# Kernel optimization log

Hardware: AMD Instinct MI355X
Metric: run time of the kernel (lower is better)

## Reference

```python
import jax, jax.numpy as jnp
import numpy as np

B, T, F, H, NH, L = 32, 512, 16, 64, 4, 2
HD = H // NH


def _ln(x, g, b, eps=1e-5):
    m = x.mean(-1, keepdims=True)
    v = ((x - m) ** 2).mean(-1, keepdims=True)
    return (x - m) / jnp.sqrt(v + eps) * g + b


def _glu(x, w, b):
    a, g = jnp.split(x @ w + b, 2, axis=-1)
    return a * jax.nn.sigmoid(g)


def _lstm_layer(x, w_ih, w_hh, b):
    # x: (B,T,H); PyTorch gate order i,f,g,o
    Bd = x.shape[0]

    def step(carry, xt):
        h, c = carry
        gates = xt @ w_ih + h @ w_hh + b
        i, f, g, o = jnp.split(gates, 4, axis=-1)
        c = jax.nn.sigmoid(f) * c + jax.nn.sigmoid(i) * jnp.tanh(g)
        h = jax.nn.sigmoid(o) * jnp.tanh(c)
        return (h, c), h

    z = jnp.zeros((Bd, H), x.dtype)
    _, hs = jax.lax.scan(step, (z, z), jnp.swapaxes(x, 0, 1))
    return jnp.swapaxes(hs, 0, 1)


def setup_inputs() -> dict:
    key = jax.random.key(0)
    specs = [
        ("x", (B, T, F), "n"),
        ("ip_w", (H,), "n"), ("ip_b", (H,), "n"),
        ("vsn_fc1_w", (F, H, H), "n"), ("vsn_fc1_b", (F, H), "n"),
        ("vsn_fc2_w", (F, H, 2 * H), "n"), ("vsn_fc2_b", (F, 2 * H), "n"),
        ("vsn_ln_g", (F, H), "1"), ("vsn_ln_b", (F, H), "0"),
        ("sel_fc1_w", (F * H, H), "n"), ("sel_fc1_b", (H,), "n"),
        ("sel_fc2_w", (H, 2 * F), "n"), ("sel_fc2_b", (2 * F,), "n"),
        ("sel_skip_w", (F * H, F), "n"), ("sel_skip_b", (F,), "n"),
        ("sel_ln_g", (F,), "1"), ("sel_ln_b", (F,), "0"),
        ("lstm_w_ih", (L, H, 4 * H), "n"), ("lstm_w_hh", (L, H, 4 * H), "n"), ("lstm_b", (L, 4 * H), "n"),
        ("plg_w", (H, 2 * H), "n"), ("plg_b", (2 * H,), "n"),
        ("pln_g", (H,), "1"), ("pln_b", (H,), "0"),
        ("qkv_w", (H, 3 * H), "n"), ("qkv_b", (3 * H,), "n"),
        ("ao_w", (H, H), "n"), ("ao_b", (H,), "n"),
        ("pag_w", (H, 2 * H), "n"), ("pag_b", (2 * H,), "n"),
        ("pan_g", (H,), "1"), ("pan_b", (H,), "0"),
        ("ff1_w", (H, 4 * H), "n"), ("ff1_b", (4 * H,), "n"),
        ("ff2_w", (4 * H, 2 * H), "n"), ("ff2_b", (2 * H,), "n"),
        ("ffln_g", (H,), "1"), ("ffln_b", (H,), "0"),
        ("fn_g", (H,), "1"), ("fn_b", (H,), "0"),
        ("out_w", (H, 1), "n"), ("out_b", (1,), "n"),
    ]
    keys = jax.random.split(key, len(specs))
    d = {}
    for (name, shp, kind), k in zip(specs, keys):
        if kind == "n":
            scale = 1.0 if name == "x" else 0.05
            d[name] = jax.random.normal(k, shp, jnp.float32) * scale
        elif kind == "1":
            d[name] = jnp.ones(shp, jnp.float32)
        else:
            d[name] = jnp.zeros(shp, jnp.float32)
    return d


def reference(x, ip_w, ip_b, vsn_fc1_w, vsn_fc1_b, vsn_fc2_w, vsn_fc2_b, vsn_ln_g, vsn_ln_b,
              sel_fc1_w, sel_fc1_b, sel_fc2_w, sel_fc2_b, sel_skip_w, sel_skip_b, sel_ln_g, sel_ln_b,
              lstm_w_ih, lstm_w_hh, lstm_b, plg_w, plg_b, pln_g, pln_b,
              qkv_w, qkv_b, ao_w, ao_b, pag_w, pag_b, pan_g, pan_b,
              ff1_w, ff1_b, ff2_w, ff2_b, ffln_g, ffln_b, fn_g, fn_b, out_w, out_b):
    Bd, Td, Fd = x.shape
    # input_proj: Linear(1,H) applied to each scalar feature -> (B,T,F,H)
    xp = x[..., None] * ip_w + ip_b
    # --- VSN (vectorized over B and T; torch loops over T and F) ---
    flat = xp.reshape(Bd, Td, Fd * H)
    h = jax.nn.elu(flat @ sel_fc1_w + sel_fc1_b)
    a, g = jnp.split(h @ sel_fc2_w + sel_fc2_b, 2, axis=-1)
    sel = _ln(a * jax.nn.sigmoid(g) + (flat @ sel_skip_w + sel_skip_b), sel_ln_g, sel_ln_b)
    w = jax.nn.softmax(sel, axis=-1)  # (B,T,F)
    h = jax.nn.elu(jnp.einsum('btfi,fio->btfo', xp, vsn_fc1_w) + vsn_fc1_b)
    a, g = jnp.split(jnp.einsum('btfi,fio->btfo', h, vsn_fc2_w) + vsn_fc2_b, 2, axis=-1)
    proc = _ln(a * jax.nn.sigmoid(g) + xp, vsn_ln_g, vsn_ln_b)  # (B,T,F,H)
    vsn_out = jnp.einsum('btf,btfh->bth', w, proc)
    # --- 2-layer LSTM encoder (dropout inactive in eval) ---
    seq = vsn_out
    for l in range(L):
        seq = _lstm_layer(seq, lstm_w_ih[l], lstm_w_hh[l], lstm_b[l])
    lo = _ln(_glu(seq, plg_w, plg_b) + vsn_out, pln_g, pln_b)
    # --- self-attention ---
    q, k, v = jnp.split(lo @ qkv_w + qkv_b, 3, axis=-1)
    q = q.reshape(Bd, Td, NH, HD)
    k = k.reshape(Bd, Td, NH, HD)
    v = v.reshape(Bd, Td, NH, HD)
    sc = jnp.einsum('bqhd,bkhd->bhqk', q, k) / jnp.sqrt(jnp.float32(HD))
    att = jnp.einsum('bhqk,bkhd->bqhd', jax.nn.softmax(sc, axis=-1), v).reshape(Bd, Td, H)
    att = att @ ao_w + ao_b
    at = _ln(_glu(att, pag_w, pag_b) + lo, pan_g, pan_b)
    # --- FF GRN + final norm ---
    h = jax.nn.elu(at @ ff1_w + ff1_b)
    a, g = jnp.split(h @ ff2_w + ff2_b, 2, axis=-1)
    ff = _ln(a * jax.nn.sigmoid(g) + at, ffln_g, ffln_b)
    ff = _ln(ff + at, fn_g, fn_b)
    return ff[:, -1, :] @ out_w + out_b  # (B, forecast_horizon)
```

## Files before the change

kernel.cpp:

```cpp
#include <hip/hip_runtime.h>
#include <math.h>


__device__ __forceinline__ float sigf(float x){
    return 1.f / (1.f + __expf(-x));
}
__device__ __forceinline__ float tanhf_(float x){
    float xc = fminf(fmaxf(x, -15.f), 15.f);
    float e = __expf(-2.f * xc);
    return (1.f - e) / (1.f + e);
}
__device__ __forceinline__ float eluf(float x){
    return x > 0.f ? x : (__expf(x) - 1.f);
}
__device__ __forceinline__ float wsum64(float v){
    #pragma unroll
    for (int o = 1; o < 64; o <<= 1) v += __shfl_xor(v, o, 64);
    return v;
}
__device__ __forceinline__ float wmax64(float v){
    #pragma unroll
    for (int o = 1; o < 64; o <<= 1) v = fmaxf(v, __shfl_xor(v, o, 64));
    return v;
}

#define BARRIER_LGKM() do {                                    \
    asm volatile("s_waitcnt lgkmcnt(0)" ::: "memory");         \
    __builtin_amdgcn_s_barrier();                              \
} while(0)

__global__ __launch_bounds__(256) void tft_vsn_kernel(
    const float* __restrict__ x,
    const float* __restrict__ ip_w, const float* __restrict__ ip_b,
    const float* __restrict__ vfc1w, const float* __restrict__ vfc1b,
    const float* __restrict__ vfc2w, const float* __restrict__ vfc2b,
    const float* __restrict__ vlng, const float* __restrict__ vlnb,
    const float* __restrict__ sfc1w, const float* __restrict__ sfc1b,
    const float* __restrict__ sfc2w, const float* __restrict__ sfc2b,
    const float* __restrict__ sskw, const float* __restrict__ sskb,
    const float* __restrict__ slng, const float* __restrict__ slnb,
    float* __restrict__ vsn_out)
{
    __shared__ __align__(16) float s_x[512];
    __shared__ __align__(16) float s_ipw[64];
    __shared__ __align__(16) float s_ipb[64];
    __shared__ __align__(16) float s_xp[32*65];
    __shared__ __align__(16) float s_W1[64*64];
    __shared__ __align__(16) float s_W2[64*128];
    __shared__ __align__(16) float s_Wsk[64*16];
    __shared__ __align__(16) float s_h[32*65];
    __shared__ __align__(16) float s_sel2[32*32];
    __shared__ __align__(16) float s_wsm[32*16];
    __shared__ __align__(16) float s_lng[64];
    __shared__ __align__(16) float s_lnb[64];
    __shared__ __align__(16) float s_b1[64];
    __shared__ __align__(16) float s_b2[128];

    const int tid  = threadIdx.x;
    const int pos0 = blockIdx.x * 32;
    const int m    = tid >> 3;
    const int g8   = tid & 7;
    const int j0   = g8 * 8;

    if (tid < 128) ((float4*)s_x)[tid] = *(const float4*)(x + pos0*16 + tid*4);
    if (tid < 64) { s_ipw[tid] = ip_w[tid]; s_ipb[tid] = ip_b[tid]; }
    __syncthreads();

    float accS[8];
    #pragma unroll
    for (int i = 0; i < 8; i++) accS[i] = 0.f;
    float accK0 = 0.f, accK1 = 0.f;

    for (int f = 0; f < 16; f++){
        {
            float xb = s_x[m*16 + f];
            #pragma unroll
            for (int i = 0; i < 8; i++)
                s_xp[m*65 + j0 + i] = xb * s_ipw[j0+i] + s_ipb[j0+i];
        }
        #pragma unroll
        for (int i = 0; i < 4; i++)
            ((float4*)s_W1)[tid + i*256] = *(const float4*)(sfc1w + f*4096 + (tid + i*256)*4);
        ((float4*)s_Wsk)[tid] = *(const float4*)(sskw + f*1024 + tid*4);
        __syncthreads();
        #pragma unroll 8
        for (int k = 0; k < 64; k++){
            float xv = s_xp[m*65 + k];
            const float4* wr = (const float4*)(s_W1 + k*64 + j0);
            float4 w0 = wr[0], w1 = wr[1];
            accS[0] += xv*w0.x; accS[1] += xv*w0.y; accS[2] += xv*w0.z; accS[3] += xv*w0.w;
            accS[4] += xv*w1.x; accS[5] += xv*w1.y; accS[6] += xv*w1.z; accS[7] += xv*w1.w;
            float2 wk = *(const float2*)(s_Wsk + k*16 + g8*2);
            accK0 += xv*wk.x; accK1 += xv*wk.y;
        }
        __syncthreads();
    }

    #pragma unroll
    for (int i = 0; i < 8; i++)
        s_h[m*65 + j0 + i] = eluf(accS[i] + sfc1b[j0+i]);
    ((float4*)s_W1)[tid]       = *(const float4*)(sfc2w + tid*4);
    ((float4*)s_W1)[tid + 256] = *(const float4*)(sfc2w + 1024 + tid*4);
    __syncthreads();

    {
        const int jj = g8 * 4;
        float a0 = 0.f, a1 = 0.f, a2 = 0.f, a3 = 0.f;
        #pragma unroll 8
        for (int k = 0; k < 64; k++){
            float hv = s_h[m*65 + k];
            float4 w = *(const float4*)(s_W1 + k*32 + jj);
            a0 += hv*w.x; a1 += hv*w.y; a2 += hv*w.z; a3 += hv*w.w;
        }
        s_sel2[m*32 + jj+0] = a0 + sfc2b[jj+0];
        s_sel2[m*32 + jj+1] = a1 + sfc2b[jj+1];
        s_sel2[m*32 + jj+2] = a2 + sfc2b[jj+2];
        s_sel2[m*32 + jj+3] = a3 + sfc2b[jj+3];
    }
    __syncthreads();

    {
        const int f0 = g8 * 2;
        float a0 = s_sel2[m*32 + f0],   g0 = s_sel2[m*32 + 16 + f0];
        float a1 = s_sel2[m*32 + f0+1], g1 = s_sel2[m*32 + 16 + f0+1];
        float pre0 = a0*sigf(g0) + accK0 + sskb[f0];
        float pre1 = a1*sigf(g1) + accK1 + sskb[f0+1];
        float sum = pre0 + pre1;
        sum += __shfl_xor(sum,1,8); sum += __shfl_xor(sum,2,8); sum += __shfl_xor(sum,4,8);
        float mean = sum * 0.0625f;
        float d0 = pre0 - mean, d1 = pre1 - mean;
        float vv = d0*d0 + d1*d1;
        vv += __shfl_xor(vv,1,8); vv += __shfl_xor(vv,2,8); vv += __shfl_xor(vv,4,8);
        float rstd = rsqrtf(vv * 0.0625f + 1e-5f);
        float sv0 = d0*rstd*slng[f0]   + slnb[f0];
        float sv1 = d1*rstd*slng[f0+1] + slnb[f0+1];
        float mx = fmaxf(sv0, sv1);
        mx = fmaxf(mx, __shfl_xor(mx,1,8));
        mx = fmaxf(mx, __shfl_xor(mx,2,8));
        mx = fmaxf(mx, __shfl_xor(mx,4,8));
        float e0 = __expf(sv0 - mx), e1 = __expf(sv1 - mx);
        float es = e0 + e1;
        es += __shfl_xor(es,1,8); es += __shfl_xor(es,2,8); es += __shfl_xor(es,4,8);
        float inv = 1.f / es;
        s_wsm[m*16 + f0]   = e0 * inv;
        s_wsm[m*16 + f0+1] = e1 * inv;
    }
    __syncthreads();

    float accV[8];
    #pragma unroll
    for (int i = 0; i < 8; i++) accV[i] = 0.f;

    for (int f = 0; f < 16; f++){
        {
            float xb = s_x[m*16 + f];
            #pragma unroll
            for (int i = 0; i < 8; i++)
                s_xp[m*65 + j0 + i] = xb * s_ipw[j0+i] + s_ipb[j0+i];
        }
        #pragma unroll
        for (int i = 0; i < 4; i++)
            ((float4*)s_W1)[tid + i*256] = *(const float4*)(vfc1w + f*4096 + (tid + i*256)*4);
        #pragma unroll
        for (int i = 0; i < 8; i++)
            ((float4*)s_W2)[tid + i*256] = *(const float4*)(vfc2w + f*8192 + (tid + i*256)*4);
        if (tid < 16)       ((float4*)s_b1)[tid]     = *(const float4*)(vfc1b + f*64  + tid*4);
        else if (tid < 48)  ((float4*)s_b2)[tid-16]  = *(const float4*)(vfc2b + f*128 + (tid-16)*4);
        else if (tid < 64)  ((float4*)s_lng)[tid-48] = *(const float4*)(vlng  + f*64  + (tid-48)*4);
        else if (tid < 80)  ((float4*)s_lnb)[tid-64] = *(const float4*)(vlnb  + f*64  + (tid-64)*4);
        __syncthreads();

        float ah[8];
        #pragma unroll
        for (int i = 0; i < 8; i++) ah[i] = 0.f;
        #pragma unroll 8
        for (int k = 0; k < 64; k++){
            float xv = s_xp[m*65 + k];
            const float4* wr = (const float4*)(s_W1 + k*64 + j0);
            float4 w0 = wr[0], w1 = wr[1];
            ah[0] += xv*w0.x; ah[1] += xv*w0.y; ah[2] += xv*w0.z; ah[3] += xv*w0.w;
            ah[4] += xv*w1.x; ah[5] += xv*w1.y; ah[6] += xv*w1.z; ah[7] += xv*w1.w;
        }
        #pragma unroll
        for (int i = 0; i < 8; i++)
            s_h[m*65 + j0 + i] = eluf(ah[i] + s_b1[j0+i]);
        __syncthreads();

        float aa[8], ag[8];
        #pragma unroll
        for (int i = 0; i < 8; i++){ aa[i] = 0.f; ag[i] = 0.f; }
        #pragma unroll 4
        for (int k = 0; k < 64; k++){
            float hv = s_h[m*65 + k];
            const float4* war = (const float4*)(s_W2 + k*128 + j0);
            const float4* wgr = (const float4*)(s_W2 + k*128 + 64 + j0);
            float4 wa0 = war[0], wa1 = war[1];
            float4 wg0 = wgr[0], wg1 = wgr[1];
            aa[0] += hv*wa0.x; aa[1] += hv*wa0.y; aa[2] += hv*wa0.z; aa[3] += hv*wa0.w;
            aa[4] += hv*wa1.x; aa[5] += hv*wa1.y; aa[6] += hv*wa1.z; aa[7] += hv*wa1.w;
            ag[0] += hv*wg0.x; ag[1] += hv*wg0.y; ag[2] += hv*wg0.z; ag[3] += hv*wg0.w;
            ag[4] += hv*wg1.x; ag[5] += hv*wg1.y; ag[6] += hv*wg1.z; ag[7] += hv*wg1.w;
        }
        float pre[8];
        float lsum = 0.f;
        #pragma unroll
        for (int i = 0; i < 8; i++){
            float av = aa[i] + s_b2[j0+i];
            float gv = ag[i] + s_b2[64 + j0+i];
            pre[i] = av * sigf(gv) + s_xp[m*65 + j0 + i];
            lsum += pre[i];
        }
        lsum += __shfl_xor(lsum,1,8); lsum += __shfl_xor(lsum,2,8); lsum += __shfl_xor(lsum,4,8);
        float mean = lsum * 0.015625f;
        float lvar = 0.f;
        #pragma unroll
        for (int i = 0; i < 8; i++){ float d = pre[i] - mean; lvar += d*d; }
        lvar += __shfl_xor(lvar,1,8); lvar += __shfl_xor(lvar,2,8); lvar += __shfl_xor(lvar,4,8);
        float rstd = rsqrtf(lvar * 0.015625f + 1e-5f);
        float wf = s_wsm[m*16 + f];
        #pragma unroll
        for (int i = 0; i < 8; i++)
            accV[i] += wf * ((pre[i] - mean) * rstd * s_lng[j0+i] + s_lnb[j0+i]);
        __syncthreads();
    }

    float4 o0 = make_float4(accV[0], accV[1], accV[2], accV[3]);
    float4 o1 = make_float4(accV[4], accV[5], accV[6], accV[7]);
    *(float4*)(vsn_out + (pos0 + m)*64 + j0)     = o0;
    *(float4*)(vsn_out + (pos0 + m)*64 + j0 + 4) = o1;
}

__global__ __launch_bounds__(256) void tft_xgates_kernel(
    const float* __restrict__ vsn, const float* __restrict__ w_ih,
    const float* __restrict__ bias, float* __restrict__ gpre)
{
    __shared__ __align__(16) float s_w[64*256];
    __shared__ __align__(16) float s_vT[64*20];
    __shared__ __align__(16) float s_b[256];
    const int tid  = threadIdx.x;
    const int pos0 = blockIdx.x * 16;

    #pragma unroll
    for (int i = 0; i < 16; i++)
        ((float4*)s_w)[tid + i*256] = *(const float4*)(w_ih + (tid + i*256)*4);
    s_b[tid] = bias[tid];
    {
        int mm = tid >> 4;
        int k0 = (tid & 15) * 4;
        float4 v = *(const float4*)(vsn + (pos0 + mm)*64 + k0);
        s_vT[(k0+0)*20 + mm] = v.x;
        s_vT[(k0+1)*20 + mm] = v.y;
        s_vT[(k0+2)*20 + mm] = v.z;
        s_vT[(k0+3)*20 + mm] = v.w;
    }
    __syncthreads();

    float acc[16];
    #pragma unroll
    for (int i = 0; i < 16; i++) acc[i] = 0.f;
    #pragma unroll 8
    for (int k = 0; k < 64; k++){
        float wv = s_w[k*256 + tid];
        const float4* vr = (const float4*)(s_vT + k*20);
        float4 v0 = vr[0], v1 = vr[1], v2 = vr[2], v3 = vr[3];
        acc[0]  += wv*v0.x; acc[1]  += wv*v0.y; acc[2]  += wv*v0.z; acc[3]  += wv*v0.w;
        acc[4]  += wv*v1.x; acc[5]  += wv*v1.y; acc[6]  += wv*v1.z; acc[7]  += wv*v1.w;
        acc[8]  += wv*v2.x; acc[9]  += wv*v2.y; acc[10] += wv*v2.z; acc[11] += wv*v2.w;
        acc[12] += wv*v3.x; acc[13] += wv*v3.y; acc[14] += wv*v3.z; acc[15] += wv*v3.w;
    }
    float bv = s_b[tid];
    #pragma unroll
    for (int i = 0; i < 16; i++)
        gpre[(pos0 + i)*256 + tid] = acc[i] + bv;
}

#define LW(P, c) make_float4((P)[(4*(c)+0)*256], (P)[(4*(c)+1)*256], \
                             (P)[(4*(c)+2)*256], (P)[(4*(c)+3)*256])

#define ACC(c, hv) { float4 h_ = (hv);                                      \
    a0  += h_.x*WA_##c.x; a0x += h_.y*WA_##c.y;                             \
    a0  += h_.z*WA_##c.z; a0x += h_.w*WA_##c.w;                             \
    a1  += h_.x*WB_##c.x; a1x += h_.y*WB_##c.y;                             \
    a1  += h_.z*WB_##c.z; a1x += h_.w*WB_##c.w; }

__global__ __launch_bounds__(512, 1) void tft_lstm_kernel(
    const float* __restrict__ w_ih, const float* __restrict__ w_hh,
    const float* __restrict__ bias, const float* __restrict__ gpre,
    float* __restrict__ seq)
{
    __shared__ __align__(16) float s_h1[2][64];
    __shared__ __align__(16) float s_h2[2][64];

    const int tid   = threadIdx.x;
    const int b     = blockIdx.x;
    const int lane  = tid & 63;
    const int wid   = tid >> 6;
    const int role  = wid >> 2;
    const int j     = ((wid & 3) << 4) | (lane & 15);
    const int kh    = (lane >> 4) & 1;
    const int gpair = (lane >> 5) & 1;
    const bool sub0 = (lane & 48) == 0;

    const int g0 = (gpair ? 64 : 0) + j;
    const int g1 = (gpair ? 192 : 128) + j;

    const float* bA;
    const float* bB;
    if (role == 0){
        bA = w_hh + (kh * 32) * 256 + g0;
        bB = w_hh + (kh * 32) * 256 + g1;
    } else {
        const float* mat = kh ? (w_hh + 16384) : (w_ih + 16384);
        bA = mat + g0;
        bB = mat + g1;
    }
    const float4 z4 = make_float4(0.f, 0.f, 0.f, 0.f);
    float4 WA_0 = LW(bA,0), WA_1 = LW(bA,1), WA_2 = LW(bA,2), WA_3 = LW(bA,3);
    float4 WA_4 = LW(bA,4), WA_5 = LW(bA,5), WA_6 = LW(bA,6), WA_7 = LW(bA,7);
    float4 WB_0 = LW(bB,0), WB_1 = LW(bB,1), WB_2 = LW(bB,2), WB_3 = LW(bB,3);
    float4 WB_4 = LW(bB,4), WB_5 = LW(bB,5), WB_6 = LW(bB,6), WB_7 = LW(bB,7);
    float4 WA_8 = z4, WA_9 = z4, WA_10 = z4, WA_11 = z4;
    float4 WA_12 = z4, WA_13 = z4, WA_14 = z4, WA_15 = z4;
    float4 WB_8 = z4, WB_9 = z4, WB_10 = z4, WB_11 = z4;
    float4 WB_12 = z4, WB_13 = z4, WB_14 = z4, WB_15 = z4;
    if (role == 1){
        WA_8  = LW(bA,8);  WA_9  = LW(bA,9);  WA_10 = LW(bA,10); WA_11 = LW(bA,11);
        WA_12 = LW(bA,12); WA_13 = LW(bA,13); WA_14 = LW(bA,14); WA_15 = LW(bA,15);
        WB_8  = LW(bB,8);  WB_9  = LW(bB,9);  WB_10 = LW(bB,10); WB_11 = LW(bB,11);
        WB_12 = LW(bB,12); WB_13 = LW(bB,13); WB_14 = LW(bB,14); WB_15 = LW(bB,15);
    }

    const float b2A = (role == 1 && kh == 0) ? bias[256 + g0] : 0.f;
    const float b2B = (role == 1 && kh == 0) ? bias[256 + g1] : 0.f;

    const bool gpl = (role == 0 && kh == 0);
    const float* gpbA = gpre + (size_t)b * 131072 + g0;
    const float* gpbB = gpre + (size_t)b * 131072 + g1;
    float gA0 = 0.f, gA1 = 0.f, gA2 = 0.f;
    float gB0 = 0.f, gB1 = 0.f, gB2 = 0.f;
    if (gpl){
        gA0 = gpbA[0];   gB0 = gpbB[0];
        gA1 = gpbA[256]; gB1 = gpbB[256];
        gA2 = gpbA[512]; gB2 = gpbB[512];
    }

    if (tid < 64){ s_h1[0][tid] = 0.f; s_h1[1][tid] = 0.f; }
    else if (tid < 128){ s_h2[0][tid-64] = 0.f; s_h2[1][tid-64] = 0.f; }
    float c_ = 0.f;
    __syncthreads();

    float* rd1 = &s_h1[1][0]; float* wr1 = &s_h1[0][0];
    float* rd2 = &s_h2[1][0]; float* wr2 = &s_h2[0][0];
    float* seqb = seq + (size_t)b * 512 * 64;

    for (int n = 0; n <= 512; ++n){
        float a0  = (role == 0) ? gA0 : b2A;
        float a1  = (role == 0) ? gB0 : b2B;
        float a0x = 0.f, a1x = 0.f;
        if (role == 0){
            const float4* hp = (const float4*)rd1 + kh * 8;
            ACC(0, hp[0]) ACC(1, hp[1]) ACC(2, hp[2]) ACC(3, hp[3])
            ACC(4, hp[4]) ACC(5, hp[5]) ACC(6, hp[6]) ACC(7, hp[7])
        } else {
            const float4* hp = (const float4*)(kh ? rd2 : rd1);
            ACC(0, hp[0])  ACC(1, hp[1])  ACC(2, hp[2])  ACC(3, hp[3])
            ACC(4, hp[4])  ACC(5, hp[5])  ACC(6, hp[6])  ACC(7, hp[7])
            ACC(8, hp[8])  ACC(9, hp[9])  ACC(10,hp[10]) ACC(11,hp[11])
            ACC(12,hp[12]) ACC(13,hp[13]) ACC(14,hp[14]) ACC(15,hp[15])
        }
        float A0 = a0 + a0x;
        float A1 = a1 + a1x;
        A0 += __shfl_xor(A0, 16, 64);
        A1 += __shfl_xor(A1, 16, 64);
        float B0 = __shfl_xor(A0, 32, 64);
        float B1 = __shfl_xor(A1, 32, 64);
        float gi = gpair ? B0 : A0;
        float gf = gpair ? A0 : B0;
        float gg = gpair ? B1 : A1;
        float go = gpair ? A1 : B1;

        if (role == 0){
            if (n < 512){
                c_ = sigf(gf)*c_ + sigf(gi)*tanhf_(gg);
                float h1v = sigf(go)*tanhf_(c_);
                if (sub0) wr1[j] = h1v;
            }
            if (gpl){
                gA0 = gA1; gA1 = gA2;
                gB0 = gB1; gB1 = gB2;
                if (n + 3 < 512){ gA2 = gpbA[(n+3)*256]; gB2 = gpbB[(n+3)*256]; }
            }
        } else if (n >= 1){
            c_ = sigf(gf)*c_ + sigf(gi)*tanhf_(gg);
            float h2v = sigf(go)*tanhf_(c_);
            if (sub0){
                wr2[j] = h2v;
                seqb[(size_t)(n-1)*64 + j] = h2v;
            }
        }
        BARRIER_LGKM();
        float* t1 = rd1; rd1 = wr1; wr1 = t1;
        float* t2 = rd2; rd2 = wr2; wr2 = t2;
    }
}

__global__ __launch_bounds__(256) void tft_lokv_kernel(
    const float* __restrict__ seq, const float* __restrict__ vsn,
    const float* __restrict__ plgw, const float* __restrict__ plgb,
    const float* __restrict__ png,  const float* __restrict__ pnb,
    const float* __restrict__ qkvw, const float* __restrict__ qkvb,
    float* __restrict__ kbuf, float* __restrict__ vbuf,
    float* __restrict__ qlast, float* __restrict__ lolast)
{
    __shared__ __align__(16) float s_pw[64*128];
    __shared__ __align__(16) float s_qw[64*192];
    __shared__ __align__(16) float s_pb[128];
    __shared__ __align__(16) float s_png[64];
    __shared__ __align__(16) float s_pnb[64];
    __shared__ __align__(16) float s_qb[192];
    __shared__ __align__(16) float s_row[4][64];
    __shared__ __align__(16) float s_lo[4][64];

    const int tid  = threadIdx.x;
    const int lane = tid & 63;
    const int wid  = tid >> 6;

    #pragma unroll
    for (int i = 0; i < 8; i++)
        ((float4*)s_pw)[tid + i*256] = *(const float4*)(plgw + (tid + i*256)*4);
    #pragma unroll
    for (int i = 0; i < 12; i++)
        ((float4*)s_qw)[tid + i*256] = *(const float4*)(qkvw + (tid + i*256)*4);
    if (tid < 128) s_pb[tid] = plgb[tid];
    if (tid < 64){ s_png[tid] = png[tid]; s_pnb[tid] = pnb[tid]; }
    if (tid < 192) s_qb[tid] = qkvb[tid];
    __syncthreads();

    for (int it = 0; it < 16; it++){
        int mpos = blockIdx.x*64 + wid*16 + it;
        int b = mpos >> 9, t = mpos & 511;
        float sv = seq[mpos*64 + lane];
        float vs = vsn[mpos*64 + lane];
        s_row[wid][lane] = sv;
        __syncthreads();
        float a = s_pb[lane], g = s_pb[64 + lane];
        #pragma unroll 8
        for (int k = 0; k < 64; k++){
            float rv = s_row[wid][k];
            a += rv * s_pw[k*128 + lane];
            g += rv * s_pw[k*128 + 64 + lane];
        }
        float pre = a * sigf(g) + vs;
        float mean = wsum64(pre) * 0.015625f;
        float d = pre - mean;
        float vv = wsum64(d*d) * 0.015625f;
        float lo = d * rsqrtf(vv + 1e-5f) * s_png[lane] + s_pnb[lane];
        s_lo[wid][lane] = lo;
        __syncthreads();
        float ka = s_qb[64 + lane], va = s_qb[128 + lane];
        #pragma unroll 8
        for (int k = 0; k < 64; k++){
            float lv = s_lo[wid][k];
            ka += lv * s_qw[k*192 + 64 + lane];
            va += lv * s_qw[k*192 + 128 + lane];
        }
        int h = lane >> 4, dd = lane & 15;
        kbuf[((b*4 + h)*512 + t)*16 + dd] = ka;
        vbuf[((b*4 + h)*512 + t)*16 + dd] = va;
        if (t == 511){
            float qa = s_qb[lane];
            #pragma unroll 8
            for (int k = 0; k < 64; k++)
                qa += s_lo[wid][k] * s_qw[k*192 + lane];
            qlast[b*64 + lane] = qa;
            lolast[b*64 + lane] = lo;
        }
    }
}

__global__ __launch_bounds__(256) void tft_head_kernel(
    const float* __restrict__ kbuf, const float* __restrict__ vbuf,
    const float* __restrict__ qlast, const float* __restrict__ lolast,
    const float* __restrict__ aow,  const float* __restrict__ aob,
    const float* __restrict__ pagw, const float* __restrict__ pagb,
    const float* __restrict__ pang, const float* __restrict__ panb,
    const float* __restrict__ ff1w, const float* __restrict__ ff1b,
    const float* __restrict__ ff2w, const float* __restrict__ ff2b,
    const float* __restrict__ fflng, const float* __restrict__ fflnb,
    const float* __restrict__ fng,  const float* __restrict__ fnb,
    const float* __restrict__ outw, const float* __restrict__ outb,
    float* __restrict__ out)
{
    __shared__ __align__(16) float s_q[64];
    __shared__ __align__(16) float s_lo[64];
    __shared__ __align__(16) float s_sc[4*512];
    __shared__ __align__(16) float s_part[4][64];
    __shared__ __align__(16) float s_a[64];
    __shared__ __align__(16) float s_a2[64];
    __shared__ __align__(16) float s_z[128];
    __shared__ __align__(16) float s_at[64];
    __shared__ __align__(16) float s_f1[256];

    const int tid = threadIdx.x;
    const int b   = blockIdx.x;
    if (tid < 64){ s_q[tid] = qlast[b*64 + tid]; s_lo[tid] = lolast[b*64 + tid]; }
    __syncthreads();

    for (int idx = tid; idx < 2048; idx += 256){
        int h = idx >> 9, t = idx & 511;
        const float4* kr = (const float4*)(kbuf + ((b*4 + h)*512 + t)*16);
        const float4* qr = (const float4*)(s_q + h*16);
        float4 k0 = kr[0], k1 = kr[1], k2 = kr[2], k3 = kr[3];
        float4 q0 = qr[0], q1 = qr[1], q2 = qr[2], q3 = qr[3];
        float d = q0.x*k0.x + q0.y*k0.y + q0.z*k0.z + q0.w*k0.w
                + q1.x*k1.x + q1.y*k1.y + q1.z*k1.z + q1.w*k1.w
                + q2.x*k2.x + q2.y*k2.y + q2.z*k2.z + q2.w*k2.w
                + q3.x*k3.x + q3.y*k3.y + q3.z*k3.z + q3.w*k3.w;
        s_sc[idx] = d * 0.25f;
    }
    __syncthreads();
    {
        int h = tid >> 6, lane = tid & 63;
        float v[8];
        float mx = -1e30f;
        #pragma unroll
        for (int j = 0; j < 8; j++){ v[j] = s_sc[h*512 + lane + j*64]; mx = fmaxf(mx, v[j]); }
        mx = wmax64(mx);
        float sum = 0.f;
        #pragma unroll
        for (int j = 0; j < 8; j++){ v[j] = __expf(v[j] - mx); sum += v[j]; }
        sum = wsum64(sum);
        float inv = 1.f / sum;
        #pragma unroll
        for (int j = 0; j < 8; j++) s_sc[h*512 + lane + j*64] = v[j] * inv;
    }
    __syncthreads();
    {
        int j = tid & 63, part = tid >> 6;
        int h = j >> 4, dd = j & 15;
        float pa = 0.f;
        for (int t = part*128; t < (part+1)*128; t++)
            pa += s_sc[h*512 + t] * vbuf[((b*4 + h)*512 + t)*16 + dd];
        s_part[part][j] = pa;
    }
    __syncthreads();
    if (tid < 64) s_a[tid] = s_part[0][tid] + s_part[1][tid] + s_part[2][tid] + s_part[3][tid];
    __syncthreads();
    if (tid < 64){
        float o = aob[tid];
        #pragma unroll 8
        for (int k = 0; k < 64; k++) o += s_a[k] * aow[k*64 + tid];
        s_a2[tid] = o;
    }
    __syncthreads();
    if (tid < 128){
        float z = pagb[tid];
        #pragma unroll 8
        for (int k = 0; k < 64; k++) z += s_a2[k] * pagw[k*128 + tid];
        s_z[tid] = z;
    }
    __syncthreads();
    if (tid < 64){
        float pre = s_z[tid] * sigf(s_z[64 + tid]) + s_lo[tid];
        float mean = wsum64(pre) * 0.015625f;
        float d = pre - mean;
        float vv = wsum64(d*d) * 0.015625f;
        s_at[tid] = d * rsqrtf(vv + 1e-5f) * pang[tid] + panb[tid];
    }
    __syncthreads();
    {
        float hv = ff1b[tid];
        #pragma unroll 8
        for (int k = 0; k < 64; k++) hv += s_at[k] * ff1w[k*256 + tid];
        s_f1[tid] = eluf(hv);
    }
    __syncthreads();
    if (tid < 128){
        float z = ff2b[tid];
        #pragma unroll 8
        for (int k = 0; k < 256; k++) z += s_f1[k] * ff2w[k*128 + tid];
        s_z[tid] = z;
    }
    __syncthreads();
    if (tid < 64){
        float pre = s_z[tid] * sigf(s_z[64 + tid]) + s_at[tid];
        float mean = wsum64(pre) * 0.015625f;
        float d = pre - mean;
        float vv = wsum64(d*d) * 0.015625f;
        float ffv = d * rsqrtf(vv + 1e-5f) * fflng[tid] + fflnb[tid];
        float pre2 = ffv + s_at[tid];
        float mean2 = wsum64(pre2) * 0.015625f;
        float d2 = pre2 - mean2;
        float v2 = wsum64(d2*d2) * 0.015625f;
        float f2 = d2 * rsqrtf(v2 + 1e-5f) * fng[tid] + fnb[tid];
        float p = wsum64(f2 * outw[tid]);
        if (tid == 0) out[b] = p + outb[0];
    }
}

extern "C" void kernel_launch(void* const* d_in, const int* in_sizes, int n_in,
                              void* d_out, int out_size, void* d_ws, size_t ws_size,
                              hipStream_t stream)
{
    const float* x     = (const float*)d_in[0];
    const float* ip_w  = (const float*)d_in[1];
    const float* ip_b  = (const float*)d_in[2];
    const float* vfc1w = (const float*)d_in[3];
    const float* vfc1b = (const float*)d_in[4];
    const float* vfc2w = (const float*)d_in[5];
    const float* vfc2b = (const float*)d_in[6];
    const float* vlng  = (const float*)d_in[7];
    const float* vlnb  = (const float*)d_in[8];
    const float* sfc1w = (const float*)d_in[9];
    const float* sfc1b = (const float*)d_in[10];
    const float* sfc2w = (const float*)d_in[11];
    const float* sfc2b = (const float*)d_in[12];
    const float* sskw  = (const float*)d_in[13];
    const float* sskb  = (const float*)d_in[14];
    const float* slng  = (const float*)d_in[15];
    const float* slnb  = (const float*)d_in[16];
    const float* lwih  = (const float*)d_in[17];
    const float* lwhh  = (const float*)d_in[18];
    const float* lb    = (const float*)d_in[19];
    const float* plgw  = (const float*)d_in[20];
    const float* plgb  = (const float*)d_in[21];
    const float* plng  = (const float*)d_in[22];
    const float* plnb  = (const float*)d_in[23];
    const float* qkvw  = (const float*)d_in[24];
    const float* qkvb  = (const float*)d_in[25];
    const float* aow   = (const float*)d_in[26];
    const float* aob   = (const float*)d_in[27];
    const float* pagw  = (const float*)d_in[28];
    const float* pagb  = (const float*)d_in[29];
    const float* pang  = (const float*)d_in[30];
    const float* panb  = (const float*)d_in[31];
    const float* ff1w  = (const float*)d_in[32];
    const float* ff1b  = (const float*)d_in[33];
    const float* ff2w  = (const float*)d_in[34];
    const float* ff2b  = (const float*)d_in[35];
    const float* fflng = (const float*)d_in[36];
    const float* fflnb = (const float*)d_in[37];
    const float* fng   = (const float*)d_in[38];
    const float* fnb   = (const float*)d_in[39];
    const float* outw  = (const float*)d_in[40];
    const float* outb  = (const float*)d_in[41];

    float* ws      = (float*)d_ws;
    float* vsn_out = ws;
    float* seq     = ws + 1048576;
    float* gpre    = ws + 2*1048576;
    float* kbuf    = ws + 6*1048576;
    float* vbuf    = ws + 7*1048576;
    float* qlast   = ws + 8*1048576;
    float* lolast  = qlast + 2048;
    float* outp    = (float*)d_out;

    tft_vsn_kernel<<<512, 256, 0, stream>>>(x, ip_w, ip_b, vfc1w, vfc1b, vfc2w, vfc2b,
                                            vlng, vlnb, sfc1w, sfc1b, sfc2w, sfc2b,
                                            sskw, sskb, slng, slnb, vsn_out);
    tft_xgates_kernel<<<1024, 256, 0, stream>>>(vsn_out, lwih, lb, gpre);
    tft_lstm_kernel<<<32, 512, 0, stream>>>(lwih, lwhh, lb, gpre, seq);
    tft_lokv_kernel<<<256, 256, 0, stream>>>(seq, vsn_out, plgw, plgb, plng, plnb,
                                             qkvw, qkvb, kbuf, vbuf, qlast, lolast);
    tft_head_kernel<<<32, 256, 0, stream>>>(kbuf, vbuf, qlast, lolast, aow, aob,
                                            pagw, pagb, pang, panb, ff1w, ff1b,
                                            ff2w, ff2b, fflng, fflnb, fng, fnb,
                                            outw, outb, outp);
}
```

Baseline: 794.2 us.

## Split LSTM layer-2 work across more wavefronts with four-way K chunks

Grows the LSTM block from 512 to 768 threads. Layer-2 now uses 8 wavefronts, each thread covering a 32-row chunk of the concatenated [w_ih; w_hh] reduction instead of 64 rows, so every thread holds the same 16 float4 weight registers and runs the same inner loop. The goal is to balance per-step latency between the layer-1 and layer-2 roles on the serial recurrence. The cost is an extra cross-lane shuffle reduction per step for layer-2 and more waves contending per CU for the barrier each timestep.

Measured after the change: 876.2 us. +10.3%, slower.

```diff
diff --git a/kernel.cpp b/kernel.cpp
--- a/kernel.cpp
+++ b/kernel.cpp
@@ -283,7 +283,7 @@
     a1  += h_.x*WB_##c.x; a1x += h_.y*WB_##c.y;                             \
     a1  += h_.z*WB_##c.z; a1x += h_.w*WB_##c.w; }
 
-__global__ __launch_bounds__(512, 1) void tft_lstm_kernel(
+__global__ __launch_bounds__(768, 1) void tft_lstm_kernel(
     const float* __restrict__ w_ih, const float* __restrict__ w_hh,
     const float* __restrict__ bias, const float* __restrict__ gpre,
     float* __restrict__ seq)
@@ -291,49 +291,44 @@
     __shared__ __align__(16) float s_h1[2][64];
     __shared__ __align__(16) float s_h2[2][64];
 
-    const int tid   = threadIdx.x;
-    const int b     = blockIdx.x;
-    const int lane  = tid & 63;
-    const int wid   = tid >> 6;
-    const int role  = wid >> 2;
-    const int j     = ((wid & 3) << 4) | (lane & 15);
-    const int kh    = (lane >> 4) & 1;
-    const int gpair = (lane >> 5) & 1;
-    const bool sub0 = (lane & 48) == 0;
-
+    const int tid  = threadIdx.x;
+    const int b    = blockIdx.x;
+    const int lane = tid & 63;
+    const int wid  = tid >> 6;
+    const bool isL2 = (wid >= 4);
+
+    int j, chunk;
+    if (!isL2){
+        j     = (wid << 4) | (lane & 15);
+        chunk = (lane >> 4) & 1;
+    } else {
+        j     = ((wid - 4) << 3) | (lane & 7);
+        chunk = (lane >> 3) & 3;
+    }
+    const int gpair = lane >> 5;
     const int g0 = (gpair ? 64 : 0) + j;
     const int g1 = (gpair ? 192 : 128) + j;
-
-    const float* bA;
-    const float* bB;
-    if (role == 0){
-        bA = w_hh + (kh * 32) * 256 + g0;
-        bB = w_hh + (kh * 32) * 256 + g1;
-    } else {
-        const float* mat = kh ? (w_hh + 16384) : (w_ih + 16384);
-        bA = mat + g0;
-        bB = mat + g1;
-    }
-    const float4 z4 = make_float4(0.f, 0.f, 0.f, 0.f);
+    const bool sub0 = isL2 ? ((lane & 0x38) == 0) : ((lane & 0x30) == 0);
+    const bool useh2 = isL2 && (chunk >= 2);
+    const int  hoff  = isL2 ? (chunk & 1) * 8 : chunk * 8;
+
+    const float* mat;
+    int row0;
+    if (!isL2){ mat = w_hh;                         row0 = chunk * 32; }
+    else      { mat = (chunk < 2) ? (w_ih + 16384)
+                                  : (w_hh + 16384); row0 = (chunk & 1) * 32; }
+    const float* bA = mat + row0 * 256 + g0;
+    const float* bB = mat + row0 * 256 + g1;
+
     float4 WA_0 = LW(bA,0), WA_1 = LW(bA,1), WA_2 = LW(bA,2), WA_3 = LW(bA,3);
     float4 WA_4 = LW(bA,4), WA_5 = LW(bA,5), WA_6 = LW(bA,6), WA_7 = LW(bA,7);
     float4 WB_0 = LW(bB,0), WB_1 = LW(bB,1), WB_2 = LW(bB,2), WB_3 = LW(bB,3);
     float4 WB_4 = LW(bB,4), WB_5 = LW(bB,5), WB_6 = LW(bB,6), WB_7 = LW(bB,7);
-    float4 WA_8 = z4, WA_9 = z4, WA_10 = z4, WA_11 = z4;
-    float4 WA_12 = z4, WA_13 = z4, WA_14 = z4, WA_15 = z4;
-    float4 WB_8 = z4, WB_9 = z4, WB_10 = z4, WB_11 = z4;
-    float4 WB_12 = z4, WB_13 = z4, WB_14 = z4, WB_15 = z4;
-    if (role == 1){
-        WA_8  = LW(bA,8);  WA_9  = LW(bA,9);  WA_10 = LW(bA,10); WA_11 = LW(bA,11);
-        WA_12 = LW(bA,12); WA_13 = LW(bA,13); WA_14 = LW(bA,14); WA_15 = LW(bA,15);
-        WB_8  = LW(bB,8);  WB_9  = LW(bB,9);  WB_10 = LW(bB,10); WB_11 = LW(bB,11);
-        WB_12 = LW(bB,12); WB_13 = LW(bB,13); WB_14 = LW(bB,14); WB_15 = LW(bB,15);
-    }
-
-    const float b2A = (role == 1 && kh == 0) ? bias[256 + g0] : 0.f;
-    const float b2B = (role == 1 && kh == 0) ? bias[256 + g1] : 0.f;
-
-    const bool gpl = (role == 0 && kh == 0);
+
+    const float b2A = (isL2 && chunk == 0) ? bias[256 + g0] : 0.f;
+    const float b2B = (isL2 && chunk == 0) ? bias[256 + g1] : 0.f;
+
+    const bool gpl = (!isL2 && chunk == 0);
     const float* gpbA = gpre + (size_t)b * 131072 + g0;
     const float* gpbB = gpre + (size_t)b * 131072 + g1;
     float gA0 = 0.f, gA1 = 0.f, gA2 = 0.f;
@@ -354,22 +349,20 @@
     float* seqb = seq + (size_t)b * 512 * 64;
 
     for (int n = 0; n <= 512; ++n){
-        float a0  = (role == 0) ? gA0 : b2A;
-        float a1  = (role == 0) ? gB0 : b2B;
+        float a0  = isL2 ? b2A : gA0;
+        float a1  = isL2 ? b2B : gB0;
         float a0x = 0.f, a1x = 0.f;
-        if (role == 0){
-            const float4* hp = (const float4*)rd1 + kh * 8;
+        {
+            const float4* hp = (const float4*)(useh2 ? rd2 : rd1) + hoff;
             ACC(0, hp[0]) ACC(1, hp[1]) ACC(2, hp[2]) ACC(3, hp[3])
             ACC(4, hp[4]) ACC(5, hp[5]) ACC(6, hp[6]) ACC(7, hp[7])
-        } else {
-            const float4* hp = (const float4*)(kh ? rd2 : rd1);
-            ACC(0, hp[0])  ACC(1, hp[1])  ACC(2, hp[2])  ACC(3, hp[3])
-            ACC(4, hp[4])  ACC(5, hp[5])  ACC(6, hp[6])  ACC(7, hp[7])
-            ACC(8, hp[8])  ACC(9, hp[9])  ACC(10,hp[10]) ACC(11,hp[11])
-            ACC(12,hp[12]) ACC(13,hp[13]) ACC(14,hp[14]) ACC(15,hp[15])
         }
         float A0 = a0 + a0x;
         float A1 = a1 + a1x;
+        if (isL2){
+            A0 += __shfl_xor(A0, 8, 64);
+            A1 += __shfl_xor(A1, 8, 64);
+        }
         A0 += __shfl_xor(A0, 16, 64);
         A1 += __shfl_xor(A1, 16, 64);
         float B0 = __shfl_xor(A0, 32, 64);
@@ -379,7 +372,7 @@
         float gg = gpair ? B1 : A1;
         float go = gpair ? A1 : B1;
 
-        if (role == 0){
+        if (!isL2){
             if (n < 512){
                 c_ = sigf(gf)*c_ + sigf(gi)*tanhf_(gg);
                 float h1v = sigf(go)*tanhf_(c_);
@@ -659,7 +652,7 @@
                                             vlng, vlnb, sfc1w, sfc1b, sfc2w, sfc2b,
                                             sskw, sskb, slng, slnb, vsn_out);
     tft_xgates_kernel<<<1024, 256, 0, stream>>>(vsn_out, lwih, lb, gpre);
-    tft_lstm_kernel<<<32, 512, 0, stream>>>(lwih, lwhh, lb, gpre, seq);
+    tft_lstm_kernel<<<32, 768, 0, stream>>>(lwih, lwhh, lb, gpre, seq);
     tft_lokv_kernel<<<256, 256, 0, stream>>>(seq, vsn_out, plgw, plgb, plng, plnb,
                                              qkvw, qkvb, kbuf, vbuf, qlast, lolast);
     tft_head_kernel<<<32, 256, 0, stream>>>(kbuf, vbuf, qlast, lolast, aow, aob,
```
